# Optimization experiments

Measured on AMD Instinct MI355X. Metric: run time of the kernel, lower is better.

The kernel has to match this reference:

```python
import jax, jax.numpy as jnp
import numpy as np

B, C, H, W = 2, 512, 64, 64
GROUPS = 32
EPS = 1e-6


def setup_inputs() -> dict:
    key = jax.random.key(0)
    ks = jax.random.split(key, 9)
    s = 1.0 / np.sqrt(C)
    return {
        "x": jax.random.normal(ks[0], (B, C, H, W), dtype=jnp.float32),
        "gamma": jnp.ones((C,), dtype=jnp.float32),
        "beta": jnp.zeros((C,), dtype=jnp.float32),
        "wq": jax.random.normal(ks[1], (C, C), dtype=jnp.float32) * s,
        "bq": jnp.zeros((C,), dtype=jnp.float32),
        "wk": jax.random.normal(ks[2], (C, C), dtype=jnp.float32) * s,
        "bk": jnp.zeros((C,), dtype=jnp.float32),
        "wv": jax.random.normal(ks[3], (C, C), dtype=jnp.float32) * s,
        "bv": jnp.zeros((C,), dtype=jnp.float32),
        "wp": jax.random.normal(ks[4], (C, C), dtype=jnp.float32) * s,
        "bp": jnp.zeros((C,), dtype=jnp.float32),
    }


def _group_norm(x, gamma, beta):
    b, c, h, w = x.shape
    xg = x.reshape(b, GROUPS, c // GROUPS, h, w)
    mean = jnp.mean(xg, axis=(2, 3, 4), keepdims=True)
    var = jnp.var(xg, axis=(2, 3, 4), keepdims=True)
    xn = ((xg - mean) * jax.lax.rsqrt(var + EPS)).reshape(b, c, h, w)
    return xn * gamma[None, :, None, None] + beta[None, :, None, None]


def reference(x, gamma, beta, wq, bq, wk, bk, wv, bv, wp, bp):
    b, c, h, w = x.shape
    hn = _group_norm(x, gamma, beta)
    # 1x1 convs == per-pixel linear; flatten spatial: (b, hw, c)
    t = hn.reshape(b, c, h * w).transpose(0, 2, 1)
    q = jnp.einsum('bnc,oc->bno', t, wq) + bq
    k = jnp.einsum('bnc,oc->bno', t, wk) + bk
    v = jnp.einsum('bnc,oc->bno', t, wv) + bv
    scale = float(int(c) ** (-0.5))
    attn = jax.nn.softmax(jnp.einsum('bic,bjc->bij', q, k) * scale, axis=-1)
    o = jnp.einsum('bij,bjc->bic', attn, v)  # (b, hw, c)
    o = jnp.einsum('bnc,oc->bno', o, wp) + bp
    o = o.transpose(0, 2, 1).reshape(b, c, h, w)
    return x + o
```

## Files before the change

kernel.cpp:

```cpp
#include <hip/hip_runtime.h>
#include <hip/hip_bf16.h>

#define B_ 2
#define C_ 512
#define HW_ 4096
#define K_ 512
#define EPS_ 1e-6f
#define SCALE_ 0.04419417382415922f
#define NEG_INF_ (-1e30f)

typedef __attribute__((ext_vector_type(8))) __bf16 bf16x8;
typedef __attribute__((ext_vector_type(4))) float f32x4;
typedef __attribute__((ext_vector_type(16))) float f32x16;

__device__ __forceinline__ unsigned short f2bf(float f) {
  union { float f; unsigned u; } v; v.f = f;
  unsigned r = v.u + 0x7fffu + ((v.u >> 16) & 1u);
  return (unsigned short)(r >> 16);
}
__device__ __forceinline__ float bf2f(unsigned short h) {
  union { unsigned u; float f; } v; v.u = ((unsigned)h) << 16;
  return v.f;
}

__device__ __forceinline__ void gld_lds16(const unsigned short* g, unsigned short* l) {
  __builtin_amdgcn_global_load_lds((const __attribute__((address_space(1))) void*)g,
                                   (__attribute__((address_space(3))) void*)l, 16, 0, 0);
}

__global__ void gn_cast(const float* __restrict__ x, float* __restrict__ stats,
                        const float* __restrict__ s0, const float* __restrict__ s1,
                        const float* __restrict__ s2, const float* __restrict__ s3,
                        unsigned short* __restrict__ dst) {
  int bid = blockIdx.x;
  int t = threadIdx.x;
  if (bid < 1024) {
    int bg = bid >> 4, row = bid & 15;
    int b = bg >> 5, g = bg & 31;
    const float* base = x + ((size_t)(b * C_ + g * 16 + row)) * HW_;
    float s = 0.f, s2 = 0.f;
    #pragma unroll
    for (int i = 0; i < 4; ++i) {
      float4 v = *reinterpret_cast<const float4*>(base + (size_t)(t + i * 256) * 4);
      s  += v.x + v.y + v.z + v.w;
      s2 += v.x * v.x + v.y * v.y + v.z * v.z + v.w * v.w;
    }
    for (int off = 32; off; off >>= 1) { s += __shfl_down(s, off); s2 += __shfl_down(s2, off); }
    __shared__ float rs[4], rs2[4];
    int w = t >> 6;
    if ((t & 63) == 0) { rs[w] = s; rs2[w] = s2; }
    __syncthreads();
    if (t == 0) {
      atomicAdd(&stats[bg], rs[0] + rs[1] + rs[2] + rs[3]);
      atomicAdd(&stats[64 + bg], rs2[0] + rs2[1] + rs2[2] + rs2[3]);
    }
  } else {
    int cid = bid - 1024;
    int which = cid >> 8, bx = cid & 255;
    const float* src = which == 0 ? s0 : which == 1 ? s1 : which == 2 ? s2 : s3;
    int i = (bx * 256 + t) * 4;
    float4 v = *reinterpret_cast<const float4*>(src + i);
    ushort4 o; o.x = f2bf(v.x); o.y = f2bf(v.y); o.z = f2bf(v.z); o.w = f2bf(v.w);
    *reinterpret_cast<ushort4*>(dst + (size_t)which * 262144 + i) = o;
  }
}

__global__ void build_t(const float* __restrict__ x, const float* __restrict__ stats,
                        const float* __restrict__ gamma, const float* __restrict__ beta,
                        unsigned short* __restrict__ tb) {
  __shared__ float lds[64 * 69];
  int n0 = blockIdx.x * 64, c0 = blockIdx.y * 64, b = blockIdx.z;
  int t = threadIdx.x;
  {
    int cl = t >> 2, ch = t & 3;
    int c = c0 + cl;
    int bg = b * 32 + (c >> 4);
    float s = stats[bg], s2v = stats[64 + bg];
    float mean = s * (1.f / 65536.f);
    float var = s2v * (1.f / 65536.f) - mean * mean;
    float rstd = rsqrtf(var + EPS_);
    float ga = gamma[c] * rstd;
    float be = beta[c] - mean * ga;
    const float* xr = x + ((size_t)(b * C_ + c)) * HW_ + n0 + ch * 16;
    #pragma unroll
    for (int i = 0; i < 4; ++i) {
      float4 v = *reinterpret_cast<const float4*>(xr + i * 4);
      int nl = ch * 16 + i * 4;
      lds[cl * 69 + nl + 0] = v.x * ga + be;
      lds[cl * 69 + nl + 1] = v.y * ga + be;
      lds[cl * 69 + nl + 2] = v.z * ga + be;
      lds[cl * 69 + nl + 3] = v.w * ga + be;
    }
  }
  __syncthreads();
  {
    int nl = t >> 2, cw = t & 3;
    unsigned short* orow = tb + ((size_t)(b * HW_ + n0 + nl)) * C_ + c0 + cw * 16;
    #pragma unroll
    for (int i = 0; i < 4; ++i) {
      ushort4 o4;
      o4.x = f2bf(lds[(cw * 16 + i * 4 + 0) * 69 + nl]);
      o4.y = f2bf(lds[(cw * 16 + i * 4 + 1) * 69 + nl]);
      o4.z = f2bf(lds[(cw * 16 + i * 4 + 2) * 69 + nl]);
      o4.w = f2bf(lds[(cw * 16 + i * 4 + 3) * 69 + nl]);
      *reinterpret_cast<ushort4*>(orow + i * 4) = o4;
    }
  }
}

__global__ __launch_bounds__(256, 2) void gemm_qkv(
    const unsigned short* __restrict__ tb, const unsigned short* __restrict__ wqkv,
    const float* __restrict__ bq, const float* __restrict__ bk, const float* __restrict__ bv,
    unsigned short* __restrict__ qb, unsigned short* __restrict__ kb,
    unsigned short* __restrict__ vTb) {
  __shared__ unsigned short Al[2][128 * 64];
  __shared__ unsigned short Bl[2][128 * 64];
  int z = blockIdx.z;
  int which = z >> 1, b = z & 1;
  const unsigned short* Ab = (which < 2) ? (tb + (size_t)b * HW_ * K_) : (wqkv + 2 * 262144);
  const unsigned short* Bb = (which < 2) ? (wqkv + which * 262144) : (tb + (size_t)b * HW_ * K_);
  int m0 = (which < 2) ? blockIdx.y * 128 : blockIdx.x * 128;
  int n0 = (which < 2) ? blockIdx.x * 128 : blockIdx.y * 128;
  int N = (which < 2) ? 512 : HW_;
  unsigned short* Cb = (which == 0) ? (qb + (size_t)b * HW_ * K_)
                     : (which == 1) ? (kb + (size_t)b * HW_ * K_)
                                    : (vTb + (size_t)b * C_ * HW_);
  const float* bias = (which == 0) ? bq : (which == 1) ? bk : bv;
  int t = threadIdx.x, lane = t & 63, w = t >> 6;
  int l15 = lane & 15, quad = lane >> 4;
  int mw = (w & 1) * 64, nw = (w >> 1) * 64;
  int sr8 = lane >> 3, sb = lane & 7;
  f32x4 acc[4][4] = {};

  #define G_STAGE(KC) do {                                                          \
    int pb = (KC) & 1;                                                              \
    _Pragma("unroll")                                                               \
    for (int q = 0; q < 4; ++q) {                                                   \
      int row = w * 32 + q * 8 + sr8;                                               \
      int gb = sb ^ (row & 7);                                                      \
      gld_lds16(Ab + (size_t)(m0 + row) * K_ + (KC) * 64 + gb * 8, &Al[pb][(w * 32 + q * 8) * 64]); \
      gld_lds16(Bb + (size_t)(n0 + row) * K_ + (KC) * 64 + gb * 8, &Bl[pb][(w * 32 + q * 8) * 64]); \
    }                                                                               \
  } while (0)

  G_STAGE(0);
  __syncthreads();
  for (int kc = 0; kc < 8; ++kc) {
    if (kc < 7) G_STAGE(kc + 1);
    const unsigned short* Ac = Al[kc & 1];
    const unsigned short* Bc = Bl[kc & 1];
    #pragma unroll
    for (int kk = 0; kk < 2; ++kk) {
      bf16x8 af[4];
      #pragma unroll
      for (int mt = 0; mt < 4; ++mt)
        af[mt] = *reinterpret_cast<const bf16x8*>(
            &Ac[(mw + mt * 16 + l15) * 64 + (((kk * 4 + quad) ^ (l15 & 7)) << 3)]);
      #pragma unroll
      for (int nt = 0; nt < 4; ++nt) {
        bf16x8 bfr = *reinterpret_cast<const bf16x8*>(
            &Bc[(nw + nt * 16 + l15) * 64 + (((kk * 4 + quad) ^ (l15 & 7)) << 3)]);
        #pragma unroll
        for (int mt = 0; mt < 4; ++mt)
          acc[mt][nt] = __builtin_amdgcn_mfma_f32_16x16x32_bf16(af[mt], bfr, acc[mt][nt], 0, 0, 0);
      }
    }
    __syncthreads();
  }
  #undef G_STAGE
  #pragma unroll
  for (int mt = 0; mt < 4; ++mt)
    #pragma unroll
    for (int nt = 0; nt < 4; ++nt)
      #pragma unroll
      for (int rr = 0; rr < 4; ++rr) {
        int row = m0 + mw + mt * 16 + quad * 4 + rr;
        int col = n0 + nw + nt * 16 + l15;
        float v = acc[mt][nt][rr] + ((which < 2) ? bias[col] : bias[row]);
        Cb[(size_t)row * N + col] = f2bf(v);
      }
}

template <int MODE>
__global__ __launch_bounds__(256, 2) void gemm_bt(
    const unsigned short* __restrict__ A, long sA,
    const unsigned short* __restrict__ B, long sB,
    void* __restrict__ Cv, long sC, int M, int N,
    const float* __restrict__ bias,
    const float* __restrict__ resid, long sR) {
  __shared__ unsigned short Al[2][128 * 64];
  __shared__ unsigned short Bl[2][128 * 64];
  int z = blockIdx.z;
  const unsigned short* Ab = A + (size_t)z * sA;
  const unsigned short* Bb = B + (size_t)z * sB;
  int n0 = blockIdx.x * 128, m0 = blockIdx.y * 128;
  int t = threadIdx.x, lane = t & 63, w = t >> 6;
  int l15 = lane & 15, quad = lane >> 4;
  int mw = (w & 1) * 64, nw = (w >> 1) * 64;
  int sr8 = lane >> 3, sb = lane & 7;
  f32x4 acc[4][4] = {};

  #define G_STAGE(KC) do {                                                          \
    int pb = (KC) & 1;                                                              \
    _Pragma("unroll")                                                               \
    for (int q = 0; q < 4; ++q) {                                                   \
      int row = w * 32 + q * 8 + sr8;                                               \
      int gb = sb ^ (row & 7);                                                      \
      gld_lds16(Ab + (size_t)(m0 + row) * K_ + (KC) * 64 + gb * 8, &Al[pb][(w * 32 + q * 8) * 64]); \
      gld_lds16(Bb + (size_t)(n0 + row) * K_ + (KC) * 64 + gb * 8, &Bl[pb][(w * 32 + q * 8) * 64]); \
    }                                                                               \
  } while (0)

  G_STAGE(0);
  __syncthreads();
  for (int kc = 0; kc < 8; ++kc) {
    if (kc < 7) G_STAGE(kc + 1);
    const unsigned short* Ac = Al[kc & 1];
    const unsigned short* Bc = Bl[kc & 1];
    #pragma unroll
    for (int kk = 0; kk < 2; ++kk) {
      bf16x8 af[4];
      #pragma unroll
      for (int mt = 0; mt < 4; ++mt)
        af[mt] = *reinterpret_cast<const bf16x8*>(
            &Ac[(mw + mt * 16 + l15) * 64 + (((kk * 4 + quad) ^ (l15 & 7)) << 3)]);
      #pragma unroll
      for (int nt = 0; nt < 4; ++nt) {
        bf16x8 bfr = *reinterpret_cast<const bf16x8*>(
            &Bc[(nw + nt * 16 + l15) * 64 + (((kk * 4 + quad) ^ (l15 & 7)) << 3)]);
        #pragma unroll
        for (int mt = 0; mt < 4; ++mt)
          acc[mt][nt] = __builtin_amdgcn_mfma_f32_16x16x32_bf16(af[mt], bfr, acc[mt][nt], 0, 0, 0);
      }
    }
    __syncthreads();
  }
  #undef G_STAGE
  #pragma unroll
  for (int mt = 0; mt < 4; ++mt)
    #pragma unroll
    for (int nt = 0; nt < 4; ++nt)
      #pragma unroll
      for (int rr = 0; rr < 4; ++rr) {
        int row = m0 + mw + mt * 16 + quad * 4 + rr;
        int col = n0 + nw + nt * 16 + l15;
        float v = acc[mt][nt][rr];
        if (MODE == 0) {
          v += bias[col];
          reinterpret_cast<unsigned short*>(Cv)[(size_t)z * sC + (size_t)row * N + col] = f2bf(v);
        } else if (MODE == 1) {
          v += bias[row];
          reinterpret_cast<unsigned short*>(Cv)[(size_t)z * sC + (size_t)row * N + col] = f2bf(v);
        } else {
          v += bias[row];
          v += resid[(size_t)z * sR + (size_t)row * N + col];
          reinterpret_cast<float*>(Cv)[(size_t)z * sC + (size_t)row * N + col] = v;
        }
      }
}

__global__ __launch_bounds__(512, 2) void attn(
    const unsigned short* __restrict__ qg, const unsigned short* __restrict__ kg,
    const unsigned short* __restrict__ vg,
    unsigned short* __restrict__ opart, float* __restrict__ mpart, float* __restrict__ lpart) {
  __shared__ unsigned short KVb[2 * 16384];
  __shared__ unsigned short Pl[64 * 264];
  __shared__ float sm_m[64], sm_l[64], sm_alpha[64], sm_red[128];
  int qt = blockIdx.x, jh = blockIdx.y, b = blockIdx.z;
  int t = threadIdx.x, lane = t & 63, w = t >> 6;
  int l15 = lane & 15, quad = lane >> 4;
  int l31 = lane & 31, hl = lane >> 5;
  int rw = w & 3, cw = w >> 2;
  int rw2 = w & 1, dg = w >> 1;
  int m0 = qt * 64;
  if (t < 64) { sm_m[t] = NEG_INF_; sm_l[t] = 0.f; }

  int st_r[4], st_kb[4];
  #pragma unroll
  for (int q = 0; q < 4; ++q) {
    int blk = w * 4 + q;
    st_r[q] = blk * 4 + (lane >> 4);
    st_kb[q] = (lane & 15) ^ (st_r[q] & 7);
  }

  #define STAGE_K(JC, KC, J0) do {                                                  \
    const unsigned short* gb = kg + ((size_t)(b * HW_ + (J0) + (JC) * 128)) * K_ + (KC) * 128; \
    unsigned short* lb = KVb + ((((JC) * 4 + (KC)) & 1) << 14);                     \
    _Pragma("unroll")                                                               \
    for (int q = 0; q < 4; ++q)                                                     \
      gld_lds16(gb + (size_t)st_r[q] * K_ + st_kb[q] * 8, lb + (w * 4 + q) * 512);  \
  } while (0)

  #define STAGE_V(DC, JC, J0) do {                                                 \
    const unsigned short* gb = vg + ((size_t)(b * K_ + (DC) * 128)) * HW_ + (J0) + (JC) * 128; \
    unsigned short* lb = KVb + (((DC) & 1) << 14);                                  \
    _Pragma("unroll")                                                               \
    for (int q = 0; q < 4; ++q)                                                     \
      gld_lds16(gb + (size_t)st_r[q] * HW_ + st_kb[q] * 8, lb + (w * 4 + q) * 512); \
  } while (0)

  bf16x8 qa[16];
  {
    const unsigned short* qrow = qg + ((size_t)(b * HW_ + m0 + rw * 16 + l15)) * K_ + quad * 8;
    #pragma unroll
    for (int kk = 0; kk < 16; ++kk)
      qa[kk] = *reinterpret_cast<const bf16x8*>(qrow + kk * 32);
  }
  f32x16 acc_o[4] = {};

  int j0 = jh * 2048;
  STAGE_K(0, 0, j0);
  __syncthreads();

  for (int it = 0; it < 8; ++it, j0 += 256) {
    f32x4 acc_s[8] = {};
    #pragma unroll
    for (int c = 0; c < 8; ++c) {
      int jc = c >> 2, kc = c & 3;
      if (c < 7) { STAGE_K((c + 1) >> 2, (c + 1) & 3, j0); }
      else       { STAGE_V(0, 0, j0); }
      const unsigned short* bufc = KVb + ((c & 1) << 14);
      __builtin_amdgcn_s_setprio(1);
      #pragma unroll
      for (int kk = 0; kk < 4; ++kk)
        #pragma unroll
        for (int ct = 0; ct < 4; ++ct) {
          int jr = cw * 64 + ct * 16 + l15;
          bf16x8 bfr = *reinterpret_cast<const bf16x8*>(
              &bufc[jr * 128 + (((kk * 4 + quad) ^ (l15 & 7)) << 3)]);
          acc_s[jc * 4 + ct] = __builtin_amdgcn_mfma_f32_16x16x32_bf16(qa[kc * 4 + kk], bfr, acc_s[jc * 4 + ct], 0, 0, 0);
        }
      __builtin_amdgcn_s_setprio(0);
      __syncthreads();
    }
    float mx[4];
    #pragma unroll
    for (int rr = 0; rr < 4; ++rr) {
      float m = NEG_INF_;
      #pragma unroll
      for (int s = 0; s < 8; ++s) {
        acc_s[s][rr] *= SCALE_;
        m = fmaxf(m, acc_s[s][rr]);
      }
      mx[rr] = m;
    }
    #pragma unroll
    for (int off = 1; off < 16; off <<= 1)
      #pragma unroll
      for (int rr = 0; rr < 4; ++rr)
        mx[rr] = fmaxf(mx[rr], __shfl_xor(mx[rr], off));
    if (l15 == 0)
      #pragma unroll
      for (int rr = 0; rr < 4; ++rr)
        sm_red[cw * 64 + rw * 16 + quad * 4 + rr] = mx[rr];
    __syncthreads();
    if (t < 64) {
      float mnew = fmaxf(sm_m[t], fmaxf(sm_red[t], sm_red[64 + t]));
      sm_alpha[t] = __expf(sm_m[t] - mnew);
      sm_m[t] = mnew;
    }
    __syncthreads();
    float sum[4] = {0.f, 0.f, 0.f, 0.f};
    #pragma unroll
    for (int s = 0; s < 8; ++s)
      #pragma unroll
      for (int rr = 0; rr < 4; ++rr) {
        int rowl = rw * 16 + quad * 4 + rr;
        float p = __expf(acc_s[s][rr] - sm_m[rowl]);
        sum[rr] += p;
        Pl[rowl * 264 + (s >> 2) * 128 + cw * 64 + (s & 3) * 16 + l15] = f2bf(p);
      }
    #pragma unroll
    for (int off = 1; off < 16; off <<= 1)
      #pragma unroll
      for (int rr = 0; rr < 4; ++rr)
        sum[rr] += __shfl_xor(sum[rr], off);
    if (l15 == 0)
      #pragma unroll
      for (int rr = 0; rr < 4; ++rr)
        sm_red[cw * 64 + rw * 16 + quad * 4 + rr] = sum[rr];
    __syncthreads();
    if (t < 64)
      sm_l[t] = sm_l[t] * sm_alpha[t] + sm_red[t] + sm_red[64 + t];
    #pragma unroll
    for (int r16 = 0; r16 < 16; ++r16) {
      int row = rw2 * 32 + (r16 & 3) + 8 * (r16 >> 2) + 4 * hl;
      float a = sm_alpha[row];
      #pragma unroll
      for (int dc = 0; dc < 4; ++dc)
        acc_o[dc][r16] *= a;
    }
    bf16x8 pa_r[8];
    #pragma unroll
    for (int c = 0; c < 8; ++c) {
      int jc = c >> 2, dc = c & 3;
      if ((c & 3) == 0) {
        #pragma unroll
        for (int ksx = 0; ksx < 8; ++ksx)
          pa_r[ksx] = *reinterpret_cast<const bf16x8*>(
              &Pl[(rw2 * 32 + l31) * 264 + jc * 128 + ksx * 16 + hl * 8]);
      }
      if (c < 7)          { STAGE_V((c + 1) & 3, (c + 1) >> 2, j0); }
      else if (it < 7)    { STAGE_K(0, 0, j0 + 256); }
      const unsigned short* bufc = KVb + ((c & 1) << 14);
      __builtin_amdgcn_s_setprio(1);
      #pragma unroll
      for (int ksx = 0; ksx < 8; ++ksx) {
        bf16x8 vb = *reinterpret_cast<const bf16x8*>(
            &bufc[(dg * 32 + l31) * 128 + (((ksx * 2 + hl) ^ (l31 & 7)) << 3)]);
        acc_o[dc] = __builtin_amdgcn_mfma_f32_32x32x16_bf16(pa_r[ksx], vb, acc_o[dc], 0, 0, 0);
      }
      __builtin_amdgcn_s_setprio(0);
      __syncthreads();
    }
  }
  #undef STAGE_K
  #undef STAGE_V
  int part = jh * 2 + b;
  unsigned short* ob = opart + ((size_t)part * HW_ + m0) * 512;
  #pragma unroll
  for (int dc = 0; dc < 4; ++dc) {
    int d = dc * 128 + dg * 32 + l31;
    #pragma unroll
    for (int r16 = 0; r16 < 16; ++r16) {
      int row = rw2 * 32 + (r16 & 3) + 8 * (r16 >> 2) + 4 * hl;
      ob[(size_t)row * 512 + d] = f2bf(acc_o[dc][r16]);
    }
  }
  if (t < 64) {
    mpart[(size_t)part * HW_ + m0 + t] = sm_m[t];
    lpart[(size_t)part * HW_ + m0 + t] = sm_l[t];
  }
}

__global__ void merge_o(const unsigned short* __restrict__ opart, const float* __restrict__ mpart,
                        const float* __restrict__ lpart, unsigned short* __restrict__ om) {
  int rg = blockIdx.x;
  int b = rg >> 12, n = rg & 4095;
  float m[2], l[2], M = NEG_INF_;
  #pragma unroll
  for (int p = 0; p < 2; ++p) {
    size_t r = (size_t)(p * 2 + b) * HW_ + n;
    m[p] = mpart[r]; l[p] = lpart[r];
    M = fmaxf(M, m[p]);
  }
  float wgt[2], L = 0.f;
  #pragma unroll
  for (int p = 0; p < 2; ++p) { wgt[p] = __expf(m[p] - M); L += l[p] * wgt[p]; }
  float inv = 1.f / L;
  int d = threadIdx.x * 2;
  float a0 = 0.f, a1 = 0.f;
  #pragma unroll
  for (int p = 0; p < 2; ++p) {
    unsigned u = *reinterpret_cast<const unsigned*>(
        &opart[((size_t)(p * 2 + b) * HW_ + n) * 512 + d]);
    a0 += bf2f((unsigned short)(u & 0xffffu)) * wgt[p];
    a1 += bf2f((unsigned short)(u >> 16)) * wgt[p];
  }
  unsigned out = (unsigned)f2bf(a0 * inv) | ((unsigned)f2bf(a1 * inv) << 16);
  *reinterpret_cast<unsigned*>(om + (size_t)rg * 512 + d) = out;
}

extern "C" void kernel_launch(void* const* d_in, const int* in_sizes, int n_in,
                              void* d_out, int out_size, void* d_ws, size_t ws_size,
                              hipStream_t stream) {
  const float* x     = (const float*)d_in[0];
  const float* gamma = (const float*)d_in[1];
  const float* beta  = (const float*)d_in[2];
  const float* wq    = (const float*)d_in[3];
  const float* bq    = (const float*)d_in[4];
  const float* wk    = (const float*)d_in[5];
  const float* bk    = (const float*)d_in[6];
  const float* wv    = (const float*)d_in[7];
  const float* bv    = (const float*)d_in[8];
  const float* wp    = (const float*)d_in[9];
  const float* bp    = (const float*)d_in[10];
  float* out = (float*)d_out;

  char* ws = (char*)d_ws;
  size_t o = 0;
  float* stats          = (float*)(ws + o);          o += 1024;
  unsigned short* tb    = (unsigned short*)(ws + o); o += 8388608;
  unsigned short* qb    = (unsigned short*)(ws + o); o += 8388608;
  unsigned short* kb    = (unsigned short*)(ws + o); o += 8388608;
  unsigned short* vTb   = (unsigned short*)(ws + o); o += 8388608;
  unsigned short* wqb   = (unsigned short*)(ws + o); o += 524288;
  unsigned short* wkb   = (unsigned short*)(ws + o); o += 524288;
  unsigned short* wvb   = (unsigned short*)(ws + o); o += 524288;
  unsigned short* wpb   = (unsigned short*)(ws + o); o += 524288;
  unsigned short* opart = (unsigned short*)(ws + o); o += 16777216;
  float* mpart          = (float*)(ws + o);          o += 65536;
  float* lpart          = (float*)(ws + o);          o += 65536;
  unsigned short* om    = tb;

  hipMemsetAsync(stats, 0, 512, stream);
  gn_cast<<<2048, 256, 0, stream>>>(x, stats, wq, wk, wv, wp, wqb);
  build_t<<<dim3(64, 8, 2), 256, 0, stream>>>(x, stats, gamma, beta, tb);
  gemm_qkv<<<dim3(4, 32, 6), 256, 0, stream>>>(tb, wqb, bq, bk, bv, qb, kb, vTb);
  attn<<<dim3(64, 2, 2), 512, 0, stream>>>(qb, kb, vTb, opart, mpart, lpart);
  merge_o<<<8192, 256, 0, stream>>>(opart, mpart, lpart, om);
  gemm_bt<2><<<dim3(32, 4, 2), 256, 0, stream>>>(wpb, 0, om, (long)HW_ * K_, out, (long)C_ * HW_, C_, HW_, bp, x, (long)C_ * HW_);
}
```

Measured before the change: 271.5 us.

## Switch QK^T to 32x32x16 MFMA tiles and reload Q fragments from global per chunk

```diff
diff --git a/kernel.cpp b/kernel.cpp
--- a/kernel.cpp
+++ b/kernel.cpp
@@ -265,13 +265,11 @@
     unsigned short* __restrict__ opart, float* __restrict__ mpart, float* __restrict__ lpart) {
   __shared__ unsigned short KVb[2 * 16384];
   __shared__ unsigned short Pl[64 * 264];
-  __shared__ float sm_m[64], sm_l[64], sm_alpha[64], sm_red[128];
+  __shared__ float sm_m[64], sm_l[64], sm_alpha[64], sm_red[256];
   int qt = blockIdx.x, jh = blockIdx.y, b = blockIdx.z;
   int t = threadIdx.x, lane = t & 63, w = t >> 6;
-  int l15 = lane & 15, quad = lane >> 4;
   int l31 = lane & 31, hl = lane >> 5;
-  int rw = w & 3, cw = w >> 2;
-  int rw2 = w & 1, dg = w >> 1;
+  int rw2 = w & 1, cw4 = w >> 1;
   int m0 = qt * 64;
   if (t < 64) { sm_m[t] = NEG_INF_; sm_l[t] = 0.f; }
 
@@ -300,88 +298,86 @@
   } while (0)
 
   bf16x8 qa[16];
-  {
-    const unsigned short* qrow = qg + ((size_t)(b * HW_ + m0 + rw * 16 + l15)) * K_ + quad * 8;
-    #pragma unroll
-    for (int kk = 0; kk < 16; ++kk)
-      qa[kk] = *reinterpret_cast<const bf16x8*>(qrow + kk * 32);
-  }
   f32x16 acc_o[4] = {};
+  f32x16 acc_s[2];
 
   int j0 = jh * 2048;
   STAGE_K(0, 0, j0);
   __syncthreads();
 
   for (int it = 0; it < 8; ++it, j0 += 256) {
-    f32x4 acc_s[8] = {};
+    acc_s[0] = (f32x16)0.f; acc_s[1] = (f32x16)0.f;
     #pragma unroll
     for (int c = 0; c < 8; ++c) {
       int jc = c >> 2, kc = c & 3;
+      if ((kc & 1) == 0) {
+        const unsigned short* qrow =
+            qg + ((size_t)(b * HW_ + m0 + rw2 * 32 + l31)) * K_ + (kc >> 1) * 256 + hl * 8;
+        #pragma unroll
+        for (int kk = 0; kk < 16; ++kk)
+          qa[kk] = *reinterpret_cast<const bf16x8*>(qrow + kk * 16);
+      }
       if (c < 7) { STAGE_K((c + 1) >> 2, (c + 1) & 3, j0); }
       else       { STAGE_V(0, 0, j0); }
       const unsigned short* bufc = KVb + ((c & 1) << 14);
       __builtin_amdgcn_s_setprio(1);
       #pragma unroll
-      for (int kk = 0; kk < 4; ++kk)
-        #pragma unroll
-        for (int ct = 0; ct < 4; ++ct) {
-          int jr = cw * 64 + ct * 16 + l15;
-          bf16x8 bfr = *reinterpret_cast<const bf16x8*>(
-              &bufc[jr * 128 + (((kk * 4 + quad) ^ (l15 & 7)) << 3)]);
-          acc_s[jc * 4 + ct] = __builtin_amdgcn_mfma_f32_16x16x32_bf16(qa[kc * 4 + kk], bfr, acc_s[jc * 4 + ct], 0, 0, 0);
-        }
+      for (int kk = 0; kk < 8; ++kk) {
+        bf16x8 bfr = *reinterpret_cast<const bf16x8*>(
+            &bufc[(cw4 * 32 + l31) * 128 + (((kk * 2 + hl) ^ (l31 & 7)) << 3)]);
+        acc_s[jc] = __builtin_amdgcn_mfma_f32_32x32x16_bf16(
+            qa[(kc & 1) * 8 + kk], bfr, acc_s[jc], 0, 0, 0);
+      }
       __builtin_amdgcn_s_setprio(0);
       __syncthreads();
     }
-    float mx[4];
-    #pragma unroll
-    for (int rr = 0; rr < 4; ++rr) {
-      float m = NEG_INF_;
-      #pragma unroll
-      for (int s = 0; s < 8; ++s) {
-        acc_s[s][rr] *= SCALE_;
-        m = fmaxf(m, acc_s[s][rr]);
-      }
-      mx[rr] = m;
-    }
-    #pragma unroll
-    for (int off = 1; off < 16; off <<= 1)
-      #pragma unroll
-      for (int rr = 0; rr < 4; ++rr)
-        mx[rr] = fmaxf(mx[rr], __shfl_xor(mx[rr], off));
-    if (l15 == 0)
-      #pragma unroll
-      for (int rr = 0; rr < 4; ++rr)
-        sm_red[cw * 64 + rw * 16 + quad * 4 + rr] = mx[rr];
+    float mx[16];
+    #pragma unroll
+    for (int r = 0; r < 16; ++r) {
+      acc_s[0][r] *= SCALE_; acc_s[1][r] *= SCALE_;
+      mx[r] = fmaxf(acc_s[0][r], acc_s[1][r]);
+    }
+    #pragma unroll
+    for (int off = 1; off < 32; off <<= 1)
+      #pragma unroll
+      for (int r = 0; r < 16; ++r)
+        mx[r] = fmaxf(mx[r], __shfl_xor(mx[r], off));
+    if (l31 == 0)
+      #pragma unroll
+      for (int r = 0; r < 16; ++r)
+        sm_red[cw4 * 64 + rw2 * 32 + (r & 3) + 8 * (r >> 2) + 4 * hl] = mx[r];
     __syncthreads();
     if (t < 64) {
-      float mnew = fmaxf(sm_m[t], fmaxf(sm_red[t], sm_red[64 + t]));
+      float mnew = fmaxf(sm_m[t],
+          fmaxf(fmaxf(sm_red[t], sm_red[64 + t]), fmaxf(sm_red[128 + t], sm_red[192 + t])));
       sm_alpha[t] = __expf(sm_m[t] - mnew);
       sm_m[t] = mnew;
     }
     __syncthreads();
-    float sum[4] = {0.f, 0.f, 0.f, 0.f};
-    #pragma unroll
-    for (int s = 0; s < 8; ++s)
-      #pragma unroll
-      for (int rr = 0; rr < 4; ++rr) {
-        int rowl = rw * 16 + quad * 4 + rr;
-        float p = __expf(acc_s[s][rr] - sm_m[rowl]);
-        sum[rr] += p;
-        Pl[rowl * 264 + (s >> 2) * 128 + cw * 64 + (s & 3) * 16 + l15] = f2bf(p);
-      }
-    #pragma unroll
-    for (int off = 1; off < 16; off <<= 1)
-      #pragma unroll
-      for (int rr = 0; rr < 4; ++rr)
-        sum[rr] += __shfl_xor(sum[rr], off);
-    if (l15 == 0)
-      #pragma unroll
-      for (int rr = 0; rr < 4; ++rr)
-        sm_red[cw * 64 + rw * 16 + quad * 4 + rr] = sum[rr];
+    float sum[16];
+    #pragma unroll
+    for (int r = 0; r < 16; ++r) {
+      int row = rw2 * 32 + (r & 3) + 8 * (r >> 2) + 4 * hl;
+      float m = sm_m[row];
+      float p0 = __expf(acc_s[0][r] - m);
+      float p1 = __expf(acc_s[1][r] - m);
+      Pl[row * 264 + cw4 * 32 + l31] = f2bf(p0);
+      Pl[row * 264 + 128 + cw4 * 32 + l31] = f2bf(p1);
+      sum[r] = p0 + p1;
+    }
+    #pragma unroll
+    for (int off = 1; off < 32; off <<= 1)
+      #pragma unroll
+      for (int r = 0; r < 16; ++r)
+        sum[r] += __shfl_xor(sum[r], off);
+    if (l31 == 0)
+      #pragma unroll
+      for (int r = 0; r < 16; ++r)
+        sm_red[cw4 * 64 + rw2 * 32 + (r & 3) + 8 * (r >> 2) + 4 * hl] = sum[r];
     __syncthreads();
     if (t < 64)
-      sm_l[t] = sm_l[t] * sm_alpha[t] + sm_red[t] + sm_red[64 + t];
+      sm_l[t] = sm_l[t] * sm_alpha[t]
+              + sm_red[t] + sm_red[64 + t] + sm_red[128 + t] + sm_red[192 + t];
     #pragma unroll
     for (int r16 = 0; r16 < 16; ++r16) {
       int row = rw2 * 32 + (r16 & 3) + 8 * (r16 >> 2) + 4 * hl;
@@ -407,7 +403,7 @@
       #pragma unroll
       for (int ksx = 0; ksx < 8; ++ksx) {
         bf16x8 vb = *reinterpret_cast<const bf16x8*>(
-            &bufc[(dg * 32 + l31) * 128 + (((ksx * 2 + hl) ^ (l31 & 7)) << 3)]);
+            &bufc[(cw4 * 32 + l31) * 128 + (((ksx * 2 + hl) ^ (l31 & 7)) << 3)]);
         acc_o[dc] = __builtin_amdgcn_mfma_f32_32x32x16_bf16(pa_r[ksx], vb, acc_o[dc], 0, 0, 0);
       }
       __builtin_amdgcn_s_setprio(0);
@@ -420,7 +416,7 @@
   unsigned short* ob = opart + ((size_t)part * HW_ + m0) * 512;
   #pragma unroll
   for (int dc = 0; dc < 4; ++dc) {
-    int d = dc * 128 + dg * 32 + l31;
+    int d = dc * 128 + cw4 * 32 + l31;
     #pragma unroll
     for (int r16 = 0; r16 < 16; ++r16) {
       int row = rw2 * 32 + (r16 & 3) + 8 * (r16 >> 2) + 4 * hl;
```

Measured after the change: 439.3 us. 1.62x slower.

## Fuse split-KV merge into output projection GEMM and drop stats memset

Applied to the files above, without the earlier changes.

```diff
diff --git a/kernel.cpp b/kernel.cpp
--- a/kernel.cpp
+++ b/kernel.cpp
@@ -28,7 +28,7 @@
                                    (__attribute__((address_space(3))) void*)l, 16, 0, 0);
 }
 
-__global__ void gn_cast(const float* __restrict__ x, float* __restrict__ stats,
+__global__ void gn_cast(const float* __restrict__ x, float* __restrict__ pstats,
                         const float* __restrict__ s0, const float* __restrict__ s1,
                         const float* __restrict__ s2, const float* __restrict__ s3,
                         unsigned short* __restrict__ dst) {
@@ -51,8 +51,8 @@
     if ((t & 63) == 0) { rs[w] = s; rs2[w] = s2; }
     __syncthreads();
     if (t == 0) {
-      atomicAdd(&stats[bg], rs[0] + rs[1] + rs[2] + rs[3]);
-      atomicAdd(&stats[64 + bg], rs2[0] + rs2[1] + rs2[2] + rs2[3]);
+      pstats[bid] = rs[0] + rs[1] + rs[2] + rs[3];
+      pstats[1024 + bid] = rs2[0] + rs2[1] + rs2[2] + rs2[3];
     }
   } else {
     int cid = bid - 1024;
@@ -65,7 +65,7 @@
   }
 }
 
-__global__ void build_t(const float* __restrict__ x, const float* __restrict__ stats,
+__global__ void build_t(const float* __restrict__ x, const float* __restrict__ pstats,
                         const float* __restrict__ gamma, const float* __restrict__ beta,
                         unsigned short* __restrict__ tb) {
   __shared__ float lds[64 * 69];
@@ -75,7 +75,12 @@
     int cl = t >> 2, ch = t & 3;
     int c = c0 + cl;
     int bg = b * 32 + (c >> 4);
-    float s = stats[bg], s2v = stats[64 + bg];
+    float s = 0.f, s2v = 0.f;
+    #pragma unroll
+    for (int r = 0; r < 16; ++r) {
+      s   += pstats[bg * 16 + r];
+      s2v += pstats[1024 + bg * 16 + r];
+    }
     float mean = s * (1.f / 65536.f);
     float var = s2v * (1.f / 65536.f) - mean * mean;
     float rstd = rsqrtf(var + EPS_);
@@ -181,18 +186,15 @@
       }
 }
 
-template <int MODE>
-__global__ __launch_bounds__(256, 2) void gemm_bt(
-    const unsigned short* __restrict__ A, long sA,
-    const unsigned short* __restrict__ B, long sB,
-    void* __restrict__ Cv, long sC, int M, int N,
-    const float* __restrict__ bias,
-    const float* __restrict__ resid, long sR) {
+__global__ __launch_bounds__(256, 2) void gemm_fin(
+    const unsigned short* __restrict__ A,
+    const unsigned short* __restrict__ opart,
+    const float* __restrict__ mpart, const float* __restrict__ lpart,
+    const float* __restrict__ bias, const float* __restrict__ resid,
+    float* __restrict__ out) {
   __shared__ unsigned short Al[2][128 * 64];
-  __shared__ unsigned short Bl[2][128 * 64];
+  __shared__ unsigned short Bl[2][128 * 68];
   int z = blockIdx.z;
-  const unsigned short* Ab = A + (size_t)z * sA;
-  const unsigned short* Bb = B + (size_t)z * sB;
   int n0 = blockIdx.x * 128, m0 = blockIdx.y * 128;
   int t = threadIdx.x, lane = t & 63, w = t >> 6;
   int l15 = lane & 15, quad = lane >> 4;
@@ -200,21 +202,61 @@
   int sr8 = lane >> 3, sb = lane & 7;
   f32x4 acc[4][4] = {};
 
-  #define G_STAGE(KC) do {                                                          \
+  float w0[4], w1[4];
+  int nrow[4];
+  #pragma unroll
+  for (int q = 0; q < 4; ++q) {
+    int n = n0 + w * 32 + q * 8 + sr8;
+    nrow[q] = n;
+    float ma = mpart[(size_t)z * HW_ + n], mb = mpart[(size_t)(2 + z) * HW_ + n];
+    float la = lpart[(size_t)z * HW_ + n], lb = lpart[(size_t)(2 + z) * HW_ + n];
+    float M = fmaxf(ma, mb);
+    float ea = __expf(ma - M), eb = __expf(mb - M);
+    float iv = 1.f / (la * ea + lb * eb);
+    w0[q] = ea * iv; w1[q] = eb * iv;
+  }
+  const unsigned short* p0 = opart + (size_t)z * HW_ * 512;
+  const unsigned short* p1 = opart + (size_t)(2 + z) * HW_ * 512;
+
+  #define STAGE_A(KC) do {                                                          \
     int pb = (KC) & 1;                                                              \
     _Pragma("unroll")                                                               \
     for (int q = 0; q < 4; ++q) {                                                   \
       int row = w * 32 + q * 8 + sr8;                                               \
       int gb = sb ^ (row & 7);                                                      \
-      gld_lds16(Ab + (size_t)(m0 + row) * K_ + (KC) * 64 + gb * 8, &Al[pb][(w * 32 + q * 8) * 64]); \
-      gld_lds16(Bb + (size_t)(n0 + row) * K_ + (KC) * 64 + gb * 8, &Bl[pb][(w * 32 + q * 8) * 64]); \
+      gld_lds16(A + (size_t)(m0 + row) * K_ + (KC) * 64 + gb * 8, &Al[pb][(w * 32 + q * 8) * 64]); \
     }                                                                               \
   } while (0)
 
-  G_STAGE(0);
+  #define STAGE_B(KC) do {                                                          \
+    int pb = (KC) & 1;                                                              \
+    _Pragma("unroll")                                                               \
+    for (int q = 0; q < 4; ++q) {                                                   \
+      int row = w * 32 + q * 8 + sr8;                                               \
+      size_t goff = (size_t)nrow[q] * 512 + (KC) * 64 + sb * 8;                     \
+      uint4 u0 = *reinterpret_cast<const uint4*>(p0 + goff);                        \
+      uint4 u1 = *reinterpret_cast<const uint4*>(p1 + goff);                        \
+      uint4 o4;                                                                     \
+      unsigned* a0 = reinterpret_cast<unsigned*>(&u0);                              \
+      unsigned* a1 = reinterpret_cast<unsigned*>(&u1);                              \
+      unsigned* od = reinterpret_cast<unsigned*>(&o4);                              \
+      _Pragma("unroll")                                                             \
+      for (int j = 0; j < 4; ++j) {                                                 \
+        float lo = bf2f((unsigned short)(a0[j] & 0xffffu)) * w0[q]                  \
+                 + bf2f((unsigned short)(a1[j] & 0xffffu)) * w1[q];                 \
+        float hi = bf2f((unsigned short)(a0[j] >> 16)) * w0[q]                      \
+                 + bf2f((unsigned short)(a1[j] >> 16)) * w1[q];                     \
+        od[j] = (unsigned)f2bf(lo) | ((unsigned)f2bf(hi) << 16);                    \
+      }                                                                             \
+      *reinterpret_cast<uint4*>(&Bl[pb][row * 68 + sb * 8]) = o4;                   \
+    }                                                                               \
+  } while (0)
+
+  STAGE_A(0);
+  STAGE_B(0);
   __syncthreads();
   for (int kc = 0; kc < 8; ++kc) {
-    if (kc < 7) G_STAGE(kc + 1);
+    if (kc < 7) { STAGE_A(kc + 1); STAGE_B(kc + 1); }
     const unsigned short* Ac = Al[kc & 1];
     const unsigned short* Bc = Bl[kc & 1];
     #pragma unroll
@@ -227,7 +269,7 @@
       #pragma unroll
       for (int nt = 0; nt < 4; ++nt) {
         bf16x8 bfr = *reinterpret_cast<const bf16x8*>(
-            &Bc[(nw + nt * 16 + l15) * 64 + (((kk * 4 + quad) ^ (l15 & 7)) << 3)]);
+            &Bc[(nw + nt * 16 + l15) * 68 + ((kk * 4 + quad) << 3)]);
         #pragma unroll
         for (int mt = 0; mt < 4; ++mt)
           acc[mt][nt] = __builtin_amdgcn_mfma_f32_16x16x32_bf16(af[mt], bfr, acc[mt][nt], 0, 0, 0);
@@ -235,7 +277,8 @@
     }
     __syncthreads();
   }
-  #undef G_STAGE
+  #undef STAGE_A
+  #undef STAGE_B
   #pragma unroll
   for (int mt = 0; mt < 4; ++mt)
     #pragma unroll
@@ -244,18 +287,8 @@
       for (int rr = 0; rr < 4; ++rr) {
         int row = m0 + mw + mt * 16 + quad * 4 + rr;
         int col = n0 + nw + nt * 16 + l15;
-        float v = acc[mt][nt][rr];
-        if (MODE == 0) {
-          v += bias[col];
-          reinterpret_cast<unsigned short*>(Cv)[(size_t)z * sC + (size_t)row * N + col] = f2bf(v);
-        } else if (MODE == 1) {
-          v += bias[row];
-          reinterpret_cast<unsigned short*>(Cv)[(size_t)z * sC + (size_t)row * N + col] = f2bf(v);
-        } else {
-          v += bias[row];
-          v += resid[(size_t)z * sR + (size_t)row * N + col];
-          reinterpret_cast<float*>(Cv)[(size_t)z * sC + (size_t)row * N + col] = v;
-        }
+        size_t idx = (size_t)z * (C_ * HW_) + (size_t)row * HW_ + col;
+        out[idx] = acc[mt][nt][rr] + bias[row] + resid[idx];
       }
 }
 
@@ -433,34 +466,6 @@
   }
 }
 
-__global__ void merge_o(const unsigned short* __restrict__ opart, const float* __restrict__ mpart,
-                        const float* __restrict__ lpart, unsigned short* __restrict__ om) {
-  int rg = blockIdx.x;
-  int b = rg >> 12, n = rg & 4095;
-  float m[2], l[2], M = NEG_INF_;
-  #pragma unroll
-  for (int p = 0; p < 2; ++p) {
-    size_t r = (size_t)(p * 2 + b) * HW_ + n;
-    m[p] = mpart[r]; l[p] = lpart[r];
-    M = fmaxf(M, m[p]);
-  }
-  float wgt[2], L = 0.f;
-  #pragma unroll
-  for (int p = 0; p < 2; ++p) { wgt[p] = __expf(m[p] - M); L += l[p] * wgt[p]; }
-  float inv = 1.f / L;
-  int d = threadIdx.x * 2;
-  float a0 = 0.f, a1 = 0.f;
-  #pragma unroll
-  for (int p = 0; p < 2; ++p) {
-    unsigned u = *reinterpret_cast<const unsigned*>(
-        &opart[((size_t)(p * 2 + b) * HW_ + n) * 512 + d]);
-    a0 += bf2f((unsigned short)(u & 0xffffu)) * wgt[p];
-    a1 += bf2f((unsigned short)(u >> 16)) * wgt[p];
-  }
-  unsigned out = (unsigned)f2bf(a0 * inv) | ((unsigned)f2bf(a1 * inv) << 16);
-  *reinterpret_cast<unsigned*>(om + (size_t)rg * 512 + d) = out;
-}
-
 extern "C" void kernel_launch(void* const* d_in, const int* in_sizes, int n_in,
                               void* d_out, int out_size, void* d_ws, size_t ws_size,
                               hipStream_t stream) {
@@ -479,7 +484,7 @@
 
   char* ws = (char*)d_ws;
   size_t o = 0;
-  float* stats          = (float*)(ws + o);          o += 1024;
+  float* pstats         = (float*)(ws + o);          o += 8192;
   unsigned short* tb    = (unsigned short*)(ws + o); o += 8388608;
   unsigned short* qb    = (unsigned short*)(ws + o); o += 8388608;
   unsigned short* kb    = (unsigned short*)(ws + o); o += 8388608;
@@ -491,13 +496,10 @@
   unsigned short* opart = (unsigned short*)(ws + o); o += 16777216;
   float* mpart          = (float*)(ws + o);          o += 65536;
   float* lpart          = (float*)(ws + o);          o += 65536;
-  unsigned short* om    = tb;
-
-  hipMemsetAsync(stats, 0, 512, stream);
-  gn_cast<<<2048, 256, 0, stream>>>(x, stats, wq, wk, wv, wp, wqb);
-  build_t<<<dim3(64, 8, 2), 256, 0, stream>>>(x, stats, gamma, beta, tb);
+
+  gn_cast<<<2048, 256, 0, stream>>>(x, pstats, wq, wk, wv, wp, wqb);
+  build_t<<<dim3(64, 8, 2), 256, 0, stream>>>(x, pstats, gamma, beta, tb);
   gemm_qkv<<<dim3(4, 32, 6), 256, 0, stream>>>(tb, wqb, bq, bk, bv, qb, kb, vTb);
   attn<<<dim3(64, 2, 2), 512, 0, stream>>>(qb, kb, vTb, opart, mpart, lpart);
-  merge_o<<<8192, 256, 0, stream>>>(opart, mpart, lpart, om);
-  gemm_bt<2><<<dim3(32, 4, 2), 256, 0, stream>>>(wpb, 0, om, (long)HW_ * K_, out, (long)C_ * HW_, C_, HW_, bp, x, (long)C_ * HW_);
-}
+  gemm_fin<<<dim3(32, 4, 2), 256, 0, stream>>>(wpb, opart, mpart, lpart, bp, x, out);
+}
```

After: 267.4 us. No clear change (-1.5%).
